# Kernel optimization log

Measured on AMD Instinct MI355X. Metric: run time of the kernel, lower is better.

Reference implementation:

```python
import jax, jax.numpy as jnp
import numpy as np


def _hard_sigmoid(x):
    # torch: clamp(0.2 * x + 0.5, 0, 1)
    return jnp.clip(0.2 * x + 0.5, 0.0, 1.0)


def _hardtanh(x):
    return jnp.clip(x, -1.0, 1.0)


def _run_dir(x, h0, c0, w_ih, w_hh, b):
    """One direction of a HardLSTM layer.
    x: [T, B, I], h0/c0: [B, H], w_ih: [4H, I], w_hh: [4H, H], b: [4H]
    (b is bias_ih + bias_hh of the original cell; identical math).
    """
    # Hoist the input projection out of the recurrence (one big GEMM).
    gx = jnp.einsum('tbi,gi->tbg', x, w_ih) + b  # [T, B, 4H]

    def step(carry, gx_t):
        h, c = carry
        gates = gx_t + h @ w_hh.T  # [B, 4H]
        i, f, g, o = jnp.split(gates, 4, axis=-1)
        i = _hard_sigmoid(i)
        f = _hard_sigmoid(f)
        g = _hardtanh(g)
        o = _hard_sigmoid(o)
        cy = f * c + i * g
        hy = o * _hardtanh(cy)
        return (hy, cy), hy

    (h, c), ys = jax.lax.scan(step, (h0, c0), gx)
    return ys, h, c


def _bidir_layer(x, h0, c0, w_ih, w_hh, b):
    """h0/c0: [2, B, H]; w_ih: [2, 4H, I]; w_hh: [2, 4H, H]; b: [2, 4H]."""
    yf, hf, cf = _run_dir(x, h0[0], c0[0], w_ih[0], w_hh[0], b[0])
    yb, hb, cb = _run_dir(x[::-1], h0[1], c0[1], w_ih[1], w_hh[1], b[1])
    yb = yb[::-1]
    # torch cat([yf.unsqueeze(2), yb.unsqueeze(2)], 2).view(T, B, 2H)
    y = jnp.concatenate([yf, yb], axis=-1)  # [T, B, 2H]
    return y, jnp.stack([hf, hb]), jnp.stack([cf, cb])


def reference(x, h0, c0, w_ih0, w_hh0, b0, w_ih1, w_hh1, b1):
    # Stacked 2-layer bidirectional HardLSTM, time-major input.
    y0, h_l0, c_l0 = _bidir_layer(x, h0[0:2], c0[0:2], w_ih0, w_hh0, b0)
    y1, h_l1, c_l1 = _bidir_layer(y0, h0[2:4], c0[2:4], w_ih1, w_hh1, b1)
    hn = jnp.concatenate([h_l0, h_l1], axis=0)  # [4, B, H]
    cn = jnp.concatenate([c_l0, c_l1], axis=0)
    return y1, hn, cn


def setup_inputs() -> dict:
    key = jax.random.key(0)
    ks = jax.random.split(key, 8)
    T, B, I, H = 512, 32, 512, 1024
    stdv = 1.0 / np.sqrt(H)  # matches reset_parameters uniform(-stdv, stdv) scale
    FGB = 1.0  # forget_gate_bias

    x = jax.random.normal(ks[0], (T, B, I), dtype=jnp.float32)
    h0 = jnp.zeros((4, B, H), dtype=jnp.float32)
    c0 = jnp.zeros((4, B, H), dtype=jnp.float32)

    def mk_w(k, shape):
        return (jax.random.normal(k, shape, dtype=jnp.float32) * stdv).astype(jnp.float32)

    w_ih0 = mk_w(ks[1], (2, 4 * H, I))
    w_hh0 = mk_w(ks[2], (2, 4 * H, H))
    b0 = mk_w(ks[3], (2, 4 * H))
    w_ih1 = mk_w(ks[4], (2, 4 * H, 2 * H))
    w_hh1 = mk_w(ks[5], (2, 4 * H, H))
    b1 = mk_w(ks[6], (2, 4 * H))
    # forget gate bias override (bias_ih forget slice = FGB, bias_hh = 0 -> sum = FGB)
    b0 = b0.at[:, H:2 * H].set(FGB)
    b1 = b1.at[:, H:2 * H].set(FGB)

    return {"x": x, "h0": h0, "c0": c0,
            "w_ih0": w_ih0, "w_hh0": w_hh0, "b0": b0,
            "w_ih1": w_ih1, "w_hh1": w_hh1, "b1": b1}
```

## Files before the change

### kernel.cpp

```cpp
#include <hip/hip_runtime.h>
#include <cstdint>


typedef _Float16 half8 __attribute__((ext_vector_type(8)));
typedef _Float16 half4v __attribute__((ext_vector_type(4)));
typedef float floatx4 __attribute__((ext_vector_type(4)));
typedef int int4v __attribute__((ext_vector_type(4)));

#define T_LEN 512
#define BATCH 32
#define HID 1024
#define NTB 16384
#define UPW 32
#define WPD 32

__device__ __forceinline__ float hsig(float x) {
  return fminf(fmaxf(fmaf(0.2f, x, 0.5f), 0.0f), 1.0f);
}
__device__ __forceinline__ float htanh(float x) {
  return fminf(fmaxf(x, -1.0f), 1.0f);
}

__device__ __forceinline__ int4v load_co16(const void* p) {
  int4v r;
  asm volatile("global_load_dwordx4 %0, %1, off sc0 sc1"
               : "=&v"(r) : "v"(p) : "memory");
  return r;
}
__device__ __forceinline__ void store_co4(void* p, int v) {
  asm volatile("global_store_dword %0, %1, off sc0 sc1"
               :: "v"(p), "v"(v) : "memory");
}
__device__ __forceinline__ void waitcnt0() {
  asm volatile("s_waitcnt vmcnt(0)" ::: "memory");
}
__device__ __forceinline__ void barrier_lgkm() {
  asm volatile("s_waitcnt lgkmcnt(0)" ::: "memory");
  __builtin_amdgcn_sched_barrier(0);
  __builtin_amdgcn_s_barrier();
  __builtin_amdgcn_sched_barrier(0);
}

__device__ __forceinline__ void gll16(const void* g, void* l) {
  __builtin_amdgcn_global_load_lds((const __attribute__((address_space(1))) void*)g,
                                   (__attribute__((address_space(3))) void*)l,
                                   16, 0, 0);
}

__device__ __forceinline__ void gate_xpose(floatx4 v, bool i1, bool i0,
                                           float& gI, float& gF,
                                           float& gG, float& gO) {
  float s0 = i1 ? v[0] : v[2], s1 = i1 ? v[1] : v[3];
  float r0 = __shfl_xor(s0, 32), r1 = __shfl_xor(s1, 32);
  float A0 = i1 ? r0 : v[0], A1 = i1 ? r1 : v[1];
  float A2 = i1 ? v[2] : r0, A3 = i1 ? v[3] : r1;
  s0 = i0 ? A0 : A1; s1 = i0 ? A2 : A3;
  r0 = __shfl_xor(s0, 16); r1 = __shfl_xor(s1, 16);
  gI = i0 ? r0 : A0; gF = i0 ? A1 : r0;
  gG = i0 ? r1 : A2; gO = i0 ? A3 : r1;
}

__device__ __forceinline__ int pack_u8_fk(int q, int fk) {
  int p = __shfl_xor(q, 16);
  int d = (fk & 1) ? ((p & 0xff) | ((q & 0xff) << 8))
                   : ((q & 0xff) | ((p & 0xff) << 8));
  int d2 = __shfl_xor(d, 32);
  return (d & 0xffff) | (d2 << 16);
}

__global__ __launch_bounds__(256) void cvt_f32_f16(const float* __restrict__ s,
                                                   _Float16* __restrict__ d,
                                                   int n4) {
  int i = blockIdx.x * blockDim.x + threadIdx.x;
  int stride = gridDim.x * blockDim.x;
  for (; i < n4; i += stride) {
    float4 v = ((const float4*)s)[i];
    half4v h = {(_Float16)v.x, (_Float16)v.y, (_Float16)v.z, (_Float16)v.w};
    ((half4v*)d)[i] = h;
  }
}

__global__ __launch_bounds__(256) void gemm_gx(const _Float16* __restrict__ A,
                                               const _Float16* __restrict__ B,
                                               const float* __restrict__ bias,
                                               _Float16* __restrict__ C,
                                               int K) {
  __shared__ __align__(16) _Float16 A_s[128 * 64];
  __shared__ __align__(16) _Float16 B_s[128 * 64];
  const int tid = threadIdx.x;
  const int lane = tid & 63;
  const int w = tid >> 6;
  const int bm = blockIdx.x >> 7;
  const int bn = blockIdx.x & 127;
  const int m0 = bm * 128, n0 = bn * 128;

  floatx4 acc[4][4] = {};

  const int srow = w * 8 + (lane >> 3);
  const int scol = ((lane & 7) ^ ((lane >> 3) & 7)) * 8;
  const _Float16* Ag = A + (size_t)(m0 + srow) * K + scol;
  const _Float16* Bg = B + (size_t)(n0 + srow) * K + scol;
  char* As_base = (char*)A_s + (size_t)(w * 8) * 128;
  char* Bs_base = (char*)B_s + (size_t)(w * 8) * 128;

  const int wm = (w >> 1) * 64;
  const int wn = (w & 1) * 64;
  const int fr = lane & 15;
  const int fk = lane >> 4;

  for (int kb = 0; kb < K; kb += 64) {
#pragma unroll
    for (int i = 0; i < 4; ++i) {
      gll16(Ag + (size_t)i * 32 * K + kb, As_base + i * 32 * 128);
      gll16(Bg + (size_t)i * 32 * K + kb, Bs_base + i * 32 * 128);
    }
    __syncthreads();
#pragma unroll
    for (int kt = 0; kt < 2; ++kt) {
      half8 af[4], bf[4];
#pragma unroll
      for (int mi = 0; mi < 4; ++mi) {
        int row = wm + mi * 16 + fr;
        int k8 = kt * 4 + fk;
        af[mi] = *(const half8*)(A_s + row * 64 + ((k8 ^ (row & 7)) << 3));
      }
#pragma unroll
      for (int ni = 0; ni < 4; ++ni) {
        int row = wn + ni * 16 + fr;
        int k8 = kt * 4 + fk;
        bf[ni] = *(const half8*)(B_s + row * 64 + ((k8 ^ (row & 7)) << 3));
      }
#pragma unroll
      for (int mi = 0; mi < 4; ++mi)
#pragma unroll
        for (int ni = 0; ni < 4; ++ni)
          acc[mi][ni] = __builtin_amdgcn_mfma_f32_16x16x32_f16(af[mi], bf[ni],
                                                               acc[mi][ni], 0, 0, 0);
    }
    __syncthreads();
  }

#pragma unroll
  for (int mi = 0; mi < 4; ++mi) {
    int rowb = m0 + wm + mi * 16 + fk * 4;
#pragma unroll
    for (int r = 0; r < 4; ++r) {
      float bv = bias[rowb + r];
#pragma unroll
      for (int ni = 0; ni < 4; ++ni) {
        int col = n0 + wn + ni * 16 + fr;
        C[(size_t)(rowb + r) * NTB + col] = (_Float16)(acc[mi][ni][r] + bv);
      }
    }
  }
}

__global__ __launch_bounds__(512, 2) void recur(const _Float16* __restrict__ gx,
                                                const _Float16* __restrict__ whh,
                                                const float* __restrict__ h0,
                                                const float* __restrict__ c0,
                                                unsigned char* __restrict__ hbuf,
                                                int* __restrict__ flags,
                                                int layer,
                                                _Float16* __restrict__ yf16,
                                                float* __restrict__ yf32,
                                                float* __restrict__ hn,
                                                float* __restrict__ cn) {
  __shared__ __align__(16) _Float16 h_s[BATCH * HID];

  const int tid = threadIdx.x;
  const int lane = tid & 63;
  const int w = tid >> 6;
  const int dir = blockIdx.x >> 5;
  const int wgd = blockIdx.x & 31;
  const int u0 = wgd * UPW;
  const int fr = lane & 15, fk = lane >> 4;

  half8 af[32];
  float rowsum = 0.f;
  {
    const int g = fr >> 2, du = fr & 3;
    const _Float16* wrow = whh + ((size_t)dir * 4096 + g * 1024 + u0 + w * 4 + du) * HID;
#pragma unroll
    for (int kt = 0; kt < 32; ++kt) {
      half8 raw = *(const half8*)(wrow + kt * 32 + fk * 8);
      half8 s;
#pragma unroll
      for (int e = 0; e < 8; ++e) {
        float v = (float)raw[e] * (1.f / 127.f);
        s[e] = (_Float16)v;
        rowsum += (float)s[e];
      }
      af[kt] = s;
    }
  }
  rowsum += __shfl_xor(rowsum, 16);
  rowsum += __shfl_xor(rowsum, 32);
  float corr0 = 1152.f * __shfl(rowsum, fk * 4 + 0);
  float corr1 = 1152.f * __shfl(rowsum, fk * 4 + 1);
  float corr2 = 1152.f * __shfl(rowsum, fk * 4 + 2);
  float corr3 = 1152.f * __shfl(rowsum, fk * 4 + 3);

  const int unit = u0 + w * 4 + fk;
  const int batA = fr, batB = 16 + fr;
  const size_t st0 = (size_t)(layer * 2 + dir) * (BATCH * HID);
  float cA = c0[st0 + (size_t)batA * HID + unit];
  float cB = c0[st0 + (size_t)batB * HID + unit];

  unsigned char* buf0 = hbuf + (size_t)dir * 32768;
  unsigned char* buf1 = hbuf + (size_t)(2 + dir) * 32768;
  int* fl = flags + dir * WPD;

  {
    float hA0 = h0[st0 + (size_t)batA * HID + unit];
    float hB0 = h0[st0 + (size_t)batB * HID + unit];
    int qA = (int)rintf(fminf(fmaxf(hA0, -1.f), 1.f) * 127.f) + 128;
    int qB = (int)rintf(fminf(fmaxf(hB0, -1.f), 1.f) * 127.f) + 128;
    int dwA = pack_u8_fk(qA, fk);
    int dwB = pack_u8_fk(qB, fk);
    if (fk == 0) {
      store_co4(buf0 + (size_t)batA * HID + u0 + w * 4, dwA);
      store_co4(buf0 + (size_t)batB * HID + u0 + w * 4, dwB);
    }
    waitcnt0();
    barrier_lgkm();
    if (tid == 0) store_co4(fl + wgd, 1);
  }

  const size_t GS = (size_t)1024 * NTB;
  const _Float16* gxp = gx + ((size_t)dir * 4096 + unit) * NTB;

  int ts0 = dir ? (T_LEN - 1) : 0;
  float gxiA = (float)gxp[0 * GS + (size_t)ts0 * BATCH + batA];
  float gxfA = (float)gxp[1 * GS + (size_t)ts0 * BATCH + batA];
  float gxgA = (float)gxp[2 * GS + (size_t)ts0 * BATCH + batA];
  float gxoA = (float)gxp[3 * GS + (size_t)ts0 * BATCH + batA];
  float gxiB = (float)gxp[0 * GS + (size_t)ts0 * BATCH + batB];
  float gxfB = (float)gxp[1 * GS + (size_t)ts0 * BATCH + batB];
  float gxgB = (float)gxp[2 * GS + (size_t)ts0 * BATCH + batB];
  float gxoB = (float)gxp[3 * GS + (size_t)ts0 * BATCH + batB];

  const bool i1 = (fk >> 1) & 1, i0 = fk & 1;
  const unsigned c64 = 0x64646464u;
  const int e = (tid + wgd * 8) & 511;
  const int eb = e >> 6, el = e & 63;

  for (int t = 0; t < T_LEN; ++t) {
    if (w == 0) {
      const int want = t + 1;
      for (;;) {
        int v;
        asm volatile("global_load_dword %0, %1, off sc0 sc1\n\ts_waitcnt vmcnt(0)"
                     : "=&v"(v) : "v"(fl + (lane & 31)) : "memory");
        if (__all(v >= want)) break;
        __builtin_amdgcn_s_sleep(2);
      }
    }
    barrier_lgkm();

    const unsigned char* src = (t & 1) ? buf1 : buf0;
    unsigned char* dst = (t & 1) ? buf0 : buf1;

    int4v u8v[4];
#pragma unroll
    for (int cc = 0; cc < 4; ++cc)
      u8v[cc] = load_co16(src + cc * 8192 + e * 16);
    waitcnt0();
#pragma unroll
    for (int cc = 0; cc < 4; ++cc) {
      int b = cc * 8 + eb;
      int lslot = el * 2;
      char* row = (char*)h_s + b * 2048;
      int swz = (b & 7) << 4;
      int4v A, B2;
      A[0]  = __builtin_amdgcn_perm(c64, (unsigned)u8v[cc][0], 0x05010400u);
      A[1]  = __builtin_amdgcn_perm(c64, (unsigned)u8v[cc][0], 0x07030602u);
      A[2]  = __builtin_amdgcn_perm(c64, (unsigned)u8v[cc][1], 0x05010400u);
      A[3]  = __builtin_amdgcn_perm(c64, (unsigned)u8v[cc][1], 0x07030602u);
      B2[0] = __builtin_amdgcn_perm(c64, (unsigned)u8v[cc][2], 0x05010400u);
      B2[1] = __builtin_amdgcn_perm(c64, (unsigned)u8v[cc][2], 0x07030602u);
      B2[2] = __builtin_amdgcn_perm(c64, (unsigned)u8v[cc][3], 0x05010400u);
      B2[3] = __builtin_amdgcn_perm(c64, (unsigned)u8v[cc][3], 0x07030602u);
      *(int4v*)(row + ((lslot * 16) ^ swz)) = A;
      *(int4v*)(row + (((lslot + 1) * 16) ^ swz)) = B2;
    }

    int tn = (t + 1 < T_LEN) ? t + 1 : t;
    int tsn = dir ? (T_LEN - 1 - tn) : tn;
    float ngxiA = (float)gxp[0 * GS + (size_t)tsn * BATCH + batA];
    float ngxfA = (float)gxp[1 * GS + (size_t)tsn * BATCH + batA];
    float ngxgA = (float)gxp[2 * GS + (size_t)tsn * BATCH + batA];
    float ngxoA = (float)gxp[3 * GS + (size_t)tsn * BATCH + batA];
    float ngxiB = (float)gxp[0 * GS + (size_t)tsn * BATCH + batB];
    float ngxfB = (float)gxp[1 * GS + (size_t)tsn * BATCH + batB];
    float ngxgB = (float)gxp[2 * GS + (size_t)tsn * BATCH + batB];
    float ngxoB = (float)gxp[3 * GS + (size_t)tsn * BATCH + batB];

    barrier_lgkm();

    floatx4 aA0 = {-corr0, -corr1, -corr2, -corr3};
    floatx4 aB0 = {-corr0, -corr1, -corr2, -corr3};
    floatx4 aA1 = {0.f, 0.f, 0.f, 0.f}, aB1 = {0.f, 0.f, 0.f, 0.f};
    {
      const char* hpA = (const char*)h_s + batA * 2048;
      const char* hpB = (const char*)h_s + batB * 2048;
      const int bxA = (batA & 7) << 4;
      const int bxB = (batB & 7) << 4;
#pragma unroll
      for (int kt = 0; kt < 32; kt += 2) {
        half8 b0A = *(const half8*)(hpA + ((kt * 64 + fk * 16) ^ bxA));
        half8 b0B = *(const half8*)(hpB + ((kt * 64 + fk * 16) ^ bxB));
        half8 b1A = *(const half8*)(hpA + (((kt + 1) * 64 + fk * 16) ^ bxA));
        half8 b1B = *(const half8*)(hpB + (((kt + 1) * 64 + fk * 16) ^ bxB));
        aA0 = __builtin_amdgcn_mfma_f32_16x16x32_f16(af[kt], b0A, aA0, 0, 0, 0);
        aB0 = __builtin_amdgcn_mfma_f32_16x16x32_f16(af[kt], b0B, aB0, 0, 0, 0);
        aA1 = __builtin_amdgcn_mfma_f32_16x16x32_f16(af[kt + 1], b1A, aA1, 0, 0, 0);
        aB1 = __builtin_amdgcn_mfma_f32_16x16x32_f16(af[kt + 1], b1B, aB1, 0, 0, 0);
      }
    }
    floatx4 vA = aA0 + aA1, vB = aB0 + aB1;

    float gI, gF, gG, gO;
    gate_xpose(vA, i1, i0, gI, gF, gG, gO);
    float igA = hsig(gI + gxiA);
    float fgA = hsig(gF + gxfA);
    float ggA = htanh(gG + gxgA);
    float ogA = hsig(gO + gxoA);
    cA = fgA * cA + igA * ggA;
    float hA = ogA * htanh(cA);

    gate_xpose(vB, i1, i0, gI, gF, gG, gO);
    float igB = hsig(gI + gxiB);
    float fgB = hsig(gF + gxfB);
    float ggB = htanh(gG + gxgB);
    float ogB = hsig(gO + gxoB);
    cB = fgB * cB + igB * ggB;
    float hB = ogB * htanh(cB);

    gxiA = ngxiA; gxfA = ngxfA; gxgA = ngxgA; gxoA = ngxoA;
    gxiB = ngxiB; gxfB = ngxfB; gxgB = ngxgB; gxoB = ngxoB;

    const int tseq = dir ? (T_LEN - 1 - t) : t;

    if (t == T_LEN - 1) {
      size_t oA = st0 + (size_t)batA * HID + unit;
      size_t oB = st0 + (size_t)batB * HID + unit;
      hn[oA] = hA; cn[oA] = cA;
      hn[oB] = hB; cn[oB] = cB;
    } else {
      int qA = (int)rintf(hA * 127.f) + 128;
      int qB = (int)rintf(hB * 127.f) + 128;
      int dwA = pack_u8_fk(qA, fk);
      int dwB = pack_u8_fk(qB, fk);
      if (fk == 0) {
        store_co4(dst + (size_t)batA * HID + u0 + w * 4, dwA);
        store_co4(dst + (size_t)batB * HID + u0 + w * 4, dwB);
      }
      waitcnt0();
      barrier_lgkm();
      if (tid == 0) store_co4(fl + wgd, t + 2);
    }

    size_t yA = ((size_t)tseq * BATCH + batA) * 2048 + (size_t)dir * 1024 + unit;
    size_t yB = ((size_t)tseq * BATCH + batB) * 2048 + (size_t)dir * 1024 + unit;
    if (yf16) { yf16[yA] = (_Float16)hA; yf16[yB] = (_Float16)hB; }
    else      { yf32[yA] = hA;           yf32[yB] = hB; }

    if (t == T_LEN - 1) {
    }
  }
}

extern "C" void kernel_launch(void* const* d_in, const int* in_sizes, int n_in,
                              void* d_out, int out_size, void* d_ws, size_t ws_size,
                              hipStream_t stream) {
  const float* x    = (const float*)d_in[0];
  const float* h0   = (const float*)d_in[1];
  const float* c0   = (const float*)d_in[2];
  const float* wih0 = (const float*)d_in[3];
  const float* whh0 = (const float*)d_in[4];
  const float* b0   = (const float*)d_in[5];
  const float* wih1 = (const float*)d_in[6];
  const float* whh1 = (const float*)d_in[7];
  const float* b1   = (const float*)d_in[8];
  float* out = (float*)d_out;

  char* ws = (char*)d_ws;
  size_t off = 0;
  int* flags = (int*)ws;                          off += 4096;
  unsigned char* hbuf = (unsigned char*)(ws + off); off += 262144;
  _Float16* xh    = (_Float16*)(ws + off);    off += (size_t)8388608 * 2;
  _Float16* wih0h = (_Float16*)(ws + off);    off += (size_t)4194304 * 2;
  _Float16* whh0h = (_Float16*)(ws + off);    off += (size_t)8388608 * 2;
  _Float16* wih1h = (_Float16*)(ws + off);    off += (size_t)16777216 * 2;
  _Float16* whh1h = (_Float16*)(ws + off);    off += (size_t)8388608 * 2;
  _Float16* y0h   = (_Float16*)(ws + off);    off += (size_t)33554432 * 2;
  _Float16* gxbuf = (_Float16*)(ws + off);    off += (size_t)134217728 * 2;

  hipMemsetAsync(flags, 0, 4096, stream);

  cvt_f32_f16<<<2048, 256, 0, stream>>>(x,    xh,    8388608 / 4);
  cvt_f32_f16<<<2048, 256, 0, stream>>>(wih0, wih0h, 4194304 / 4);
  cvt_f32_f16<<<2048, 256, 0, stream>>>(whh0, whh0h, 8388608 / 4);
  cvt_f32_f16<<<2048, 256, 0, stream>>>(wih1, wih1h, 16777216 / 4);
  cvt_f32_f16<<<2048, 256, 0, stream>>>(whh1, whh1h, 8388608 / 4);

  float* hn = out + 33554432;
  float* cn = out + 33685504;

  gemm_gx<<<8192, 256, 0, stream>>>(wih0h, xh, b0, gxbuf, 512);
  recur<<<64, 512, 0, stream>>>(gxbuf, whh0h, h0, c0, hbuf, flags, 0,
                                y0h, nullptr, hn, cn);
  gemm_gx<<<8192, 256, 0, stream>>>(wih1h, y0h, b1, gxbuf, 2048);
  recur<<<64, 512, 0, stream>>>(gxbuf, whh1h, h0, c0, hbuf + 131072, flags + 128, 1,
                                nullptr, out, hn, cn);
}
```

Baseline: 5.719 ms.

## Stage hidden-state output in LDS and publish it with one coalesced store per workgroup

Each workgroup now gathers its quantized hidden-state bytes in a small LDS buffer. A single wave then writes them to the exchange buffer as one contiguous 1KB block of 16-byte stores, replacing many scattered 4-byte stores from every wave. The exchange buffer layout changes to workgroup-major, and the consumer's unpack indexing is updated to match. This also means only wave 0 waits on its stores before setting the flag, which adds a block barrier and an LDS round trip on the critical path.

```diff
diff --git a/kernel.cpp b/kernel.cpp
--- a/kernel.cpp
+++ b/kernel.cpp
@@ -26,6 +26,10 @@
   asm volatile("global_load_dwordx4 %0, %1, off sc0 sc1"
                : "=&v"(r) : "v"(p) : "memory");
   return r;
+}
+__device__ __forceinline__ void store_co16(void* p, int4v v) {
+  asm volatile("global_store_dwordx4 %0, %1, off sc0 sc1"
+               :: "v"(p), "v"(v) : "memory");
 }
 __device__ __forceinline__ void store_co4(void* p, int v) {
   asm volatile("global_store_dword %0, %1, off sc0 sc1"
@@ -155,18 +159,21 @@
   }
 }
 
-__global__ __launch_bounds__(512, 2) void recur(const _Float16* __restrict__ gx,
-                                                const _Float16* __restrict__ whh,
-                                                const float* __restrict__ h0,
-                                                const float* __restrict__ c0,
-                                                unsigned char* __restrict__ hbuf,
-                                                int* __restrict__ flags,
-                                                int layer,
-                                                _Float16* __restrict__ yf16,
-                                                float* __restrict__ yf32,
-                                                float* __restrict__ hn,
-                                                float* __restrict__ cn) {
+__global__
+__attribute__((amdgpu_flat_work_group_size(512, 512), amdgpu_waves_per_eu(2, 2)))
+void recur(const _Float16* __restrict__ gx,
+           const _Float16* __restrict__ whh,
+           const float* __restrict__ h0,
+           const float* __restrict__ c0,
+           unsigned char* __restrict__ hbuf,
+           int* __restrict__ flags,
+           int layer,
+           _Float16* __restrict__ yf16,
+           float* __restrict__ yf32,
+           float* __restrict__ hn,
+           float* __restrict__ cn) {
   __shared__ __align__(16) _Float16 h_s[BATCH * HID];
+  __shared__ __align__(16) int hout_s[BATCH * 8];
 
   const int tid = threadIdx.x;
   const int lane = tid & 63;
@@ -186,10 +193,10 @@
       half8 raw = *(const half8*)(wrow + kt * 32 + fk * 8);
       half8 s;
 #pragma unroll
-      for (int e = 0; e < 8; ++e) {
-        float v = (float)raw[e] * (1.f / 127.f);
-        s[e] = (_Float16)v;
-        rowsum += (float)s[e];
+      for (int e2 = 0; e2 < 8; ++e2) {
+        float v = (float)raw[e2] * (1.f / 127.f);
+        s[e2] = (_Float16)v;
+        rowsum += (float)s[e2];
       }
       af[kt] = s;
     }
@@ -219,12 +226,16 @@
     int dwA = pack_u8_fk(qA, fk);
     int dwB = pack_u8_fk(qB, fk);
     if (fk == 0) {
-      store_co4(buf0 + (size_t)batA * HID + u0 + w * 4, dwA);
-      store_co4(buf0 + (size_t)batB * HID + u0 + w * 4, dwB);
-    }
-    waitcnt0();
+      hout_s[batA * 8 + w] = dwA;
+      hout_s[batB * 8 + w] = dwB;
+    }
     barrier_lgkm();
-    if (tid == 0) store_co4(fl + wgd, 1);
+    if (w == 0) {
+      int4v v = *(const int4v*)((const char*)hout_s + lane * 16);
+      store_co16(buf0 + (size_t)wgd * 1024 + lane * 16, v);
+      waitcnt0();
+      if (lane == 0) store_co4(fl + wgd, 1);
+    }
   }
 
   const size_t GS = (size_t)1024 * NTB;
@@ -243,7 +254,6 @@
   const bool i1 = (fk >> 1) & 1, i0 = fk & 1;
   const unsigned c64 = 0x64646464u;
   const int e = (tid + wgd * 8) & 511;
-  const int eb = e >> 6, el = e & 63;
 
   for (int t = 0; t < T_LEN; ++t) {
     if (w == 0) {
@@ -264,14 +274,18 @@
     int4v u8v[4];
 #pragma unroll
     for (int cc = 0; cc < 4; ++cc)
-      u8v[cc] = load_co16(src + cc * 8192 + e * 16);
+      u8v[cc] = load_co16(src + (size_t)(cc * 512 + e) * 16);
     waitcnt0();
 #pragma unroll
     for (int cc = 0; cc < 4; ++cc) {
-      int b = cc * 8 + eb;
-      int lslot = el * 2;
-      char* row = (char*)h_s + b * 2048;
-      int swz = (b & 7) << 4;
+      int chunk = cc * 512 + e;
+      int wg2 = chunk >> 6;
+      int rc = chunk & 63;
+      int bat = rc >> 1;
+      int U = wg2 * 32 + (rc & 1) * 16;
+      char* row = (char*)h_s + bat * 2048;
+      int swz = (bat & 7) << 4;
+      int lslot = U >> 3;
       int4v A, B2;
       A[0]  = __builtin_amdgcn_perm(c64, (unsigned)u8v[cc][0], 0x05010400u);
       A[1]  = __builtin_amdgcn_perm(c64, (unsigned)u8v[cc][0], 0x07030602u);
@@ -353,21 +367,22 @@
       int dwA = pack_u8_fk(qA, fk);
       int dwB = pack_u8_fk(qB, fk);
       if (fk == 0) {
-        store_co4(dst + (size_t)batA * HID + u0 + w * 4, dwA);
-        store_co4(dst + (size_t)batB * HID + u0 + w * 4, dwB);
-      }
-      waitcnt0();
+        hout_s[batA * 8 + w] = dwA;
+        hout_s[batB * 8 + w] = dwB;
+      }
       barrier_lgkm();
-      if (tid == 0) store_co4(fl + wgd, t + 2);
+      if (w == 0) {
+        int4v v = *(const int4v*)((const char*)hout_s + lane * 16);
+        store_co16(dst + (size_t)wgd * 1024 + lane * 16, v);
+        waitcnt0();
+        if (lane == 0) store_co4(fl + wgd, t + 2);
+      }
     }
 
     size_t yA = ((size_t)tseq * BATCH + batA) * 2048 + (size_t)dir * 1024 + unit;
     size_t yB = ((size_t)tseq * BATCH + batB) * 2048 + (size_t)dir * 1024 + unit;
     if (yf16) { yf16[yA] = (_Float16)hA; yf16[yB] = (_Float16)hB; }
     else      { yf32[yA] = hA;           yf32[yB] = hB; }
-
-    if (t == T_LEN - 1) {
-    }
   }
 }
 
```

Result: slower. 6.669 ms (+16.6%).
